# Performance work log

Hardware: AMD Instinct MI355X
Metric: run time of the kernel (lower is better)

Reference implementation:

```python
import jax, jax.numpy as jnp
import numpy as np

B, S, DM, H, DK, DV = 2, 2048, 1024, 16, 64, 64

def setup_inputs() -> dict:
    key = jax.random.key(0)
    ks = jax.random.split(key, 12)
    s = 0.02
    return {
        "Q": jax.random.normal(ks[0], (B, S, DM), jnp.float32),
        "K": jax.random.normal(ks[1], (B, S, DM), jnp.float32),
        "V": jax.random.normal(ks[2], (B, S, DM), jnp.float32),
        "mask": jax.random.randint(ks[3], (B, S, S), 0, 2).astype(bool),
        "wq": jax.random.normal(ks[4], (DM, H * DK), jnp.float32) * s,
        "bq": jnp.zeros((H * DK,), jnp.float32),
        "wk": jax.random.normal(ks[5], (DM, H * DK), jnp.float32) * s,
        "bk": jnp.zeros((H * DK,), jnp.float32),
        "wv": jax.random.normal(ks[6], (DM, H * DV), jnp.float32) * s,
        "bv": jnp.zeros((H * DV,), jnp.float32),
        "wo": jax.random.normal(ks[7], (H * DV, DM), jnp.float32) * s,
        "bo": jnp.zeros((DM,), jnp.float32),
    }

def reference(Q, K, V, mask, wq, bq, wk, bk, wv, bv, wo, bo):
    b = Q.shape[0]
    # projections -> [b, h, s, d]
    q = (Q @ wq + bq).reshape(b, -1, H, DK).transpose(0, 2, 1, 3)
    k = (K @ wk + bk).reshape(b, -1, H, DK).transpose(0, 2, 1, 3)
    v = (V @ wv + bv).reshape(b, -1, H, DV).transpose(0, 2, 1, 3)
    # scaled dot-product attention with boolean mask (True = masked out)
    scores = jnp.einsum("bhqd,bhkd->bhqk", q, k) / jnp.sqrt(jnp.float32(DK))
    scores = jnp.where(mask[:, None, :, :], jnp.float32(-1e9), scores)
    attn = jax.nn.softmax(scores, axis=-1)  # [b,h,s,s]
    ctx = jnp.einsum("bhqk,bhkd->bhqd", attn, v)
    ctx = ctx.transpose(0, 2, 1, 3).reshape(b, -1, H * DV)
    out = ctx @ wo + bo  # [b, s, d_model]
    return out, attn
```

## Files before the change

### kernel.cpp

```cpp
#include <hip/hip_runtime.h>

typedef unsigned short u16;
typedef unsigned int u32;
typedef unsigned long long u64;
typedef __attribute__((ext_vector_type(8))) short bf16x8;
typedef __attribute__((ext_vector_type(4))) float f32x4;

#define NB 2
#define NS 2048
#define NDM 1024
#define NH 16

#define MFMA_B16(a, b, c) __builtin_amdgcn_mfma_f32_16x16x32_bf16(a, b, c, 0, 0, 0)

__device__ __forceinline__ u16 f2bf(float f) {
  union { float f; unsigned u; } v; v.f = f;
  return (u16)((v.u + 0x7fffu + ((v.u >> 16) & 1u)) >> 16);
}
__device__ __forceinline__ float bf2f(u16 h) {
  union { float f; unsigned u; } v; v.u = ((u32)h) << 16; return v.f;
}

__global__ __launch_bounds__(256) void cast3_bf16(const float* __restrict__ a,
                                                  const float* __restrict__ b,
                                                  const float* __restrict__ c,
                                                  u16* __restrict__ oa, u16* __restrict__ ob,
                                                  u16* __restrict__ oc) {
  int i = blockIdx.x * 256 + threadIdx.x;
  const float* src; u16* dst; int j;
  if (i < 1048576) { src = a; dst = oa; j = i; }
  else if (i < 2097152) { src = b; dst = ob; j = i - 1048576; }
  else { src = c; dst = oc; j = i - 2097152; }
  const float4 v = reinterpret_cast<const float4*>(src)[j];
  ushort4 o; o.x = f2bf(v.x); o.y = f2bf(v.y); o.z = f2bf(v.z); o.w = f2bf(v.w);
  reinterpret_cast<ushort4*>(dst)[j] = o;
}

struct TW4 { const float* in[4]; u16* out[4]; };
__global__ __launch_bounds__(256) void transpose_w4(TW4 tw) {
  __shared__ float tile[32][33];
  const float* in = tw.in[blockIdx.z];
  u16* out = tw.out[blockIdx.z];
  int bx = blockIdx.x, by = blockIdx.y;
  int x = threadIdx.x & 31, y0 = threadIdx.x >> 5;
#pragma unroll
  for (int i = 0; i < 4; i++) {
    int y = y0 + i * 8;
    tile[y][x] = in[(by * 32 + y) * NDM + bx * 32 + x];
  }
  __syncthreads();
#pragma unroll
  for (int i = 0; i < 4; i++) {
    int y = y0 + i * 8;
    out[(bx * 32 + y) * NDM + by * 32 + x] = f2bf(tile[x][y]);
  }
}

__global__ __launch_bounds__(256) void mask2bits(const u32* __restrict__ mask, u32* __restrict__ mb) {
  int idx = blockIdx.x * 256 + threadIdx.x;
  u32 mw0 = mask[threadIdx.x & 63];
  bool floatmode = (__ballot(mw0 == 0x3F800000u) != 0ull);
  bool bytemode = !floatmode && (__ballot((mw0 >> 8) != 0u) != 0ull);
  int row = idx >> 6;
  int wword = idx & 63;
  u32 bits = 0;
  if (!bytemode) {
    const uint4* p = reinterpret_cast<const uint4*>(mask + (size_t)row * 2048 + wword * 32);
#pragma unroll
    for (int i = 0; i < 8; i++) {
      uint4 v = p[i];
      bits |= (v.x ? 1u : 0u) << (i * 4 + 0);
      bits |= (v.y ? 1u : 0u) << (i * 4 + 1);
      bits |= (v.z ? 1u : 0u) << (i * 4 + 2);
      bits |= (v.w ? 1u : 0u) << (i * 4 + 3);
    }
  } else {
    const uint4* p = reinterpret_cast<const uint4*>(
        reinterpret_cast<const unsigned char*>(mask) + (size_t)row * 2048 + wword * 32);
#pragma unroll
    for (int i = 0; i < 2; i++) {
      uint4 v = p[i];
      u32 wsv[4] = {v.x, v.y, v.z, v.w};
#pragma unroll
      for (int j = 0; j < 4; j++)
#pragma unroll
        for (int kq = 0; kq < 4; kq++)
          bits |= ((((wsv[j] >> (kq * 8)) & 0xffu) != 0u) ? 1u : 0u) << (i * 16 + j * 4 + kq);
    }
  }
  mb[idx] = bits;
}

struct GArgs { const u16* X; const u16* W; const float* bias; void* out; int mode; float scale; };

__global__ __launch_bounds__(256, 2) void gemm_bt(GArgs g0, GArgs g1, GArgs g2) {
  GArgs ga = (blockIdx.z == 0) ? g0 : (blockIdx.z == 1 ? g1 : g2);
  const int K = 1024, N = 1024;
  __shared__ u16 As[128 * 32];
  __shared__ u16 Bs[128 * 32];
  const int t = threadIdx.x, w = t >> 6, l = t & 63;
  const int m0 = blockIdx.x * 128, n0 = blockIdx.y * 128;
  const int wm = (w >> 1) * 64, wn = (w & 1) * 64;
  const f32x4 fz = {0.f, 0.f, 0.f, 0.f};
  f32x4 acc[4][4];
#pragma unroll
  for (int i = 0; i < 4; i++)
#pragma unroll
    for (int j = 0; j < 4; j++) acc[i][j] = fz;

  for (int k0 = 0; k0 < K; k0 += 32) {
#pragma unroll
    for (int i = 0; i < 2; i++) {
      int idx = i * 256 + w * 64 + l;
      int r = idx >> 2, c = (idx & 3) * 8;
      __builtin_amdgcn_global_load_lds(
          reinterpret_cast<const unsigned*>(ga.X + (size_t)(m0 + r) * K + k0 + c),
          reinterpret_cast<unsigned*>(&As[(i * 256 + w * 64) * 8]), 16, 0, 0);
      __builtin_amdgcn_global_load_lds(
          reinterpret_cast<const unsigned*>(ga.W + (size_t)(n0 + r) * K + k0 + c),
          reinterpret_cast<unsigned*>(&Bs[(i * 256 + w * 64) * 8]), 16, 0, 0);
    }
    __syncthreads();
    bf16x8 af[4], bfr[4];
#pragma unroll
    for (int mt = 0; mt < 4; mt++)
      af[mt] = *reinterpret_cast<const bf16x8*>(&As[(wm + mt * 16 + (l & 15)) * 32 + (l >> 4) * 8]);
#pragma unroll
    for (int nt = 0; nt < 4; nt++)
      bfr[nt] = *reinterpret_cast<const bf16x8*>(&Bs[(wn + nt * 16 + (l & 15)) * 32 + (l >> 4) * 8]);
#pragma unroll
    for (int mt = 0; mt < 4; mt++)
#pragma unroll
      for (int nt = 0; nt < 4; nt++)
        acc[mt][nt] = MFMA_B16(af[mt], bfr[nt], acc[mt][nt]);
    __syncthreads();
  }

#pragma unroll
  for (int nt = 0; nt < 4; nt++) {
    int n = n0 + wn + nt * 16 + (l & 15);
    float bias = ga.bias[n];
#pragma unroll
    for (int mt = 0; mt < 4; mt++) {
      int mb = m0 + wm + mt * 16 + ((l >> 4) << 2);
#pragma unroll
      for (int r = 0; r < 4; r++) {
        int m = mb + r;
        float v = (acc[mt][nt][r] + bias) * ga.scale;
        if (ga.mode == 2) {
          reinterpret_cast<float*>(ga.out)[(size_t)m * N + n] = v;
        } else {
          int b = m >> 11, s = m & 2047, h = n >> 6, d = n & 63;
          if (ga.mode == 0)
            reinterpret_cast<u16*>(ga.out)[(((size_t)(b * NH + h) * NS + s) << 6) + d] = f2bf(v);
          else
            reinterpret_cast<u16*>(ga.out)[((size_t)(b * NH + h) * 64 + d) * NS + s] = f2bf(v);
        }
      }
    }
  }
}

__global__ __launch_bounds__(256, 4) void attn_kernel(
    const u16* __restrict__ qh, const u16* __restrict__ kh, const u16* __restrict__ vT,
    const u32* __restrict__ mb, float* __restrict__ attn, u16* __restrict__ ctx) {
  __shared__ u16 Ks[2][32 * 64];
  __shared__ u16 Vs[3][64 * 32];
  __shared__ u16 Ps[4][2][16 * 40];
  const int tid = threadIdx.x, w = tid >> 6, l = tid & 63;
  int id = blockIdx.x;
  int wgid = (id & 7) * 128 + (id >> 3);
  int qt = wgid & 31, pr = wgid >> 5;
  int h = pr & 15, b = pr >> 4;
  const size_t head = (size_t)b * NH + h;
  const u16* qp = qh + head * NS * 64;
  const u16* kp = kh + head * NS * 64;
  const u16* vp = vT + head * 64 * NS;
  const int qr0 = qt * 64 + w * 16;
  const int lo = l & 15, hi = l >> 4;
  const int rbase = hi << 2;
  const f32x4 fz = {0.f, 0.f, 0.f, 0.f};

  bf16x8 aq0, aq1;
  {
    const u16* p = qp + (size_t)(qr0 + lo) * 64 + hi * 8;
    aq0 = *reinterpret_cast<const bf16x8*>(p);
    aq1 = *reinterpret_cast<const bf16x8*>(p + 32);
  }
  const u32* mrow = mb + ((size_t)b * NS + qr0 + rbase) * 64;

  const int k_row = tid >> 3, k_slot = tid & 7;
  const u16* ksrc0 = kp + (size_t)k_row * 64 + ((k_slot ^ (k_row & 7)) * 8);
  const int v_dv = tid >> 2, v_slot = tid & 3;
  const u16* vsrc0 = vp + (size_t)v_dv * NS + ((v_slot ^ ((v_dv >> 1) & 3)) * 8);
  const int sxk = lo & 7;
  const int sxv = (lo >> 1) & 3;

#define STAGE_KT(tt, bi)                                                                \
  __builtin_amdgcn_global_load_lds(                                                     \
      reinterpret_cast<const unsigned*>(ksrc0 + (size_t)(tt) * 2048),                   \
      reinterpret_cast<unsigned*>(&Ks[bi][w * 512]), 16, 0, 0);
#define STAGE_VT(tt, bi)                                                                \
  __builtin_amdgcn_global_load_lds(                                                     \
      reinterpret_cast<const unsigned*>(vsrc0 + (size_t)(tt) * 32),                     \
      reinterpret_cast<unsigned*>(&Vs[bi][w * 512]), 16, 0, 0);

#define QK_TILE(kb, s0, s1)                                                             \
  {                                                                                     \
    const u16* kbase = &Ks[kb][0];                                                      \
    bf16x8 b00 = *reinterpret_cast<const bf16x8*>(&kbase[(lo) * 64 + ((hi ^ sxk) * 8)]);        \
    bf16x8 b01 = *reinterpret_cast<const bf16x8*>(&kbase[(lo) * 64 + (((4 + hi) ^ sxk) * 8)]);  \
    bf16x8 b10 = *reinterpret_cast<const bf16x8*>(&kbase[(16 + lo) * 64 + ((hi ^ sxk) * 8)]);   \
    bf16x8 b11 = *reinterpret_cast<const bf16x8*>(&kbase[(16 + lo) * 64 + (((4 + hi) ^ sxk) * 8)]); \
    s0 = MFMA_B16(aq1, b01, MFMA_B16(aq0, b00, fz));                                    \
    s1 = MFMA_B16(aq1, b11, MFMA_B16(aq0, b10, fz));                                    \
  }
#define EXP_PS(pb, s0, s1)                                                              \
  {                                                                                     \
    u16* pc = &Ps[w][pb][0];                                                            \
    float p;                                                                            \
    p = ((mc0 >> lo) & 1u) ? 0.f : __expf(s0[0]) * rs0; pc[(rbase + 0) * 40 + lo] = f2bf(p); \
    p = ((mc1 >> lo) & 1u) ? 0.f : __expf(s0[1]) * rs1; pc[(rbase + 1) * 40 + lo] = f2bf(p); \
    p = ((mc2 >> lo) & 1u) ? 0.f : __expf(s0[2]) * rs2; pc[(rbase + 2) * 40 + lo] = f2bf(p); \
    p = ((mc3 >> lo) & 1u) ? 0.f : __expf(s0[3]) * rs3; pc[(rbase + 3) * 40 + lo] = f2bf(p); \
    int bit1 = 16 + lo;                                                                 \
    p = ((mc0 >> bit1) & 1u) ? 0.f : __expf(s1[0]) * rs0; pc[(rbase + 0) * 40 + 16 + lo] = f2bf(p); \
    p = ((mc1 >> bit1) & 1u) ? 0.f : __expf(s1[1]) * rs1; pc[(rbase + 1) * 40 + 16 + lo] = f2bf(p); \
    p = ((mc2 >> bit1) & 1u) ? 0.f : __expf(s1[2]) * rs2; pc[(rbase + 2) * 40 + 16 + lo] = f2bf(p); \
    p = ((mc3 >> bit1) & 1u) ? 0.f : __expf(s1[3]) * rs3; pc[(rbase + 3) * 40 + 16 + lo] = f2bf(p); \
  }
#define PV_STORES(tt, pb, vb)                                                           \
  {                                                                                     \
    u16* pp = &Ps[w][pb][0];                                                            \
    const u16* vbase = &Vs[vb][0];                                                      \
    bf16x8 pa = *reinterpret_cast<const bf16x8*>(&pp[lo * 40 + hi * 8]);                \
    bf16x8 v0 = *reinterpret_cast<const bf16x8*>(&vbase[(lo) * 32 + ((hi ^ sxv) * 8)]);        \
    bf16x8 v1 = *reinterpret_cast<const bf16x8*>(&vbase[(16 + lo) * 32 + ((hi ^ sxv) * 8)]);   \
    bf16x8 v2 = *reinterpret_cast<const bf16x8*>(&vbase[(32 + lo) * 32 + ((hi ^ sxv) * 8)]);   \
    bf16x8 v3 = *reinterpret_cast<const bf16x8*>(&vbase[(48 + lo) * 32 + ((hi ^ sxv) * 8)]);   \
    c0 = MFMA_B16(pa, v0, c0);                                                          \
    c1 = MFMA_B16(pa, v1, c1);                                                          \
    c2 = MFMA_B16(pa, v2, c2);                                                          \
    c3 = MFMA_B16(pa, v3, c3);                                                          \
    float* arow = abase + (size_t)srow * NS + (tt) * 32 + schunk * 8;                   \
    bf16x8 q0 = *reinterpret_cast<const bf16x8*>(&pp[srow * 40 + schunk * 8]);          \
    f32x4 o0, o1;                                                                       \
    _Pragma("unroll") for (int j = 0; j < 4; ++j) {                                     \
      o0[j] = bf2f((u16)q0[j]); o1[j] = bf2f((u16)q0[j + 4]);                           \
    }                                                                                   \
    *reinterpret_cast<f32x4*>(arow + 0) = o0;                                           \
    *reinterpret_cast<f32x4*>(arow + 4) = o1;                                           \
  }

  float rs0 = 0.f, rs1 = 0.f, rs2 = 0.f, rs3 = 0.f;

  u32 mc0 = mrow[0], mc1 = mrow[64], mc2 = mrow[128], mc3 = mrow[192];
  STAGE_KT(0, 0);
  asm volatile("s_waitcnt vmcnt(0)" ::: "memory");
  __builtin_amdgcn_s_barrier();
  asm volatile("" ::: "memory");

  for (int t = 0; t < 64; ++t) {
    STAGE_KT(t + 1, (t + 1) & 1);
    u32 mn0 = mrow[t + 1], mn1 = mrow[65 + t], mn2 = mrow[129 + t], mn3 = mrow[193 + t];
    asm volatile("" ::: "memory");
    f32x4 s0, s1;
    QK_TILE(t & 1, s0, s1);
    rs0 += ((mc0 >> lo) & 1u) ? 0.f : __expf(s0[0]);
    rs1 += ((mc1 >> lo) & 1u) ? 0.f : __expf(s0[1]);
    rs2 += ((mc2 >> lo) & 1u) ? 0.f : __expf(s0[2]);
    rs3 += ((mc3 >> lo) & 1u) ? 0.f : __expf(s0[3]);
    int bit1 = 16 + lo;
    rs0 += ((mc0 >> bit1) & 1u) ? 0.f : __expf(s1[0]);
    rs1 += ((mc1 >> bit1) & 1u) ? 0.f : __expf(s1[1]);
    rs2 += ((mc2 >> bit1) & 1u) ? 0.f : __expf(s1[2]);
    rs3 += ((mc3 >> bit1) & 1u) ? 0.f : __expf(s1[3]);
    mc0 = mn0; mc1 = mn1; mc2 = mn2; mc3 = mn3;
    asm volatile("s_waitcnt vmcnt(4)" ::: "memory");
    __builtin_amdgcn_s_barrier();
    asm volatile("" ::: "memory");
  }

  {
    float v;
    v = rs0; v += __shfl_xor(v, 1); v += __shfl_xor(v, 2); v += __shfl_xor(v, 4); v += __shfl_xor(v, 8);
    rs0 = 1.f / fmaxf(v, 1e-30f);
    v = rs1; v += __shfl_xor(v, 1); v += __shfl_xor(v, 2); v += __shfl_xor(v, 4); v += __shfl_xor(v, 8);
    rs1 = 1.f / fmaxf(v, 1e-30f);
    v = rs2; v += __shfl_xor(v, 1); v += __shfl_xor(v, 2); v += __shfl_xor(v, 4); v += __shfl_xor(v, 8);
    rs2 = 1.f / fmaxf(v, 1e-30f);
    v = rs3; v += __shfl_xor(v, 1); v += __shfl_xor(v, 2); v += __shfl_xor(v, 4); v += __shfl_xor(v, 8);
    rs3 = 1.f / fmaxf(v, 1e-30f);
  }

  f32x4 c0 = fz, c1 = fz, c2 = fz, c3 = fz;
  float* abase = attn + (head * NS + qr0) * NS;
  const int srow = l >> 2, schunk = l & 3;

  mc0 = mrow[0]; mc1 = mrow[64]; mc2 = mrow[128]; mc3 = mrow[192];
  STAGE_KT(0, 0);
  STAGE_VT(0, 0);
  asm volatile("s_waitcnt vmcnt(0)" ::: "memory");
  __builtin_amdgcn_s_barrier();
  asm volatile("" ::: "memory");

  {
    STAGE_KT(1, 1);
    STAGE_VT(1, 1);
    u32 mn0 = mrow[1], mn1 = mrow[65], mn2 = mrow[129], mn3 = mrow[193];
    asm volatile("" ::: "memory");
    f32x4 s0, s1;
    QK_TILE(0, s0, s1);
    EXP_PS(0, s0, s1);
    mc0 = mn0; mc1 = mn1; mc2 = mn2; mc3 = mn3;
    asm volatile("s_waitcnt vmcnt(4)" ::: "memory");
    __builtin_amdgcn_s_barrier();
    asm volatile("" ::: "memory");
  }

  for (int t = 1; t < 64; ++t) {
    if (t + 1 < 64) {
      int vb2 = (t + 1) % 3;
      STAGE_KT(t + 1, (t + 1) & 1);
      STAGE_VT(t + 1, vb2);
    }
    u32 mn0 = mrow[t + 1], mn1 = mrow[65 + t], mn2 = mrow[129 + t], mn3 = mrow[193 + t];
    asm volatile("" ::: "memory");
    PV_STORES(t - 1, (t - 1) & 1, (t - 1) % 3);
    f32x4 s0, s1;
    QK_TILE(t & 1, s0, s1);
    EXP_PS(t & 1, s0, s1);
    mc0 = mn0; mc1 = mn1; mc2 = mn2; mc3 = mn3;
    asm volatile("s_waitcnt vmcnt(6)" ::: "memory");
    __builtin_amdgcn_s_barrier();
    asm volatile("" ::: "memory");
  }

  PV_STORES(63, 1, 0);

#define CTXW(cv, ct)                                                                      \
  {                                                                                       \
    ctx[((size_t)b * NS + qr0 + rbase + 0) * 1024 + h * 64 + (ct)*16 + lo] = f2bf(cv[0]); \
    ctx[((size_t)b * NS + qr0 + rbase + 1) * 1024 + h * 64 + (ct)*16 + lo] = f2bf(cv[1]); \
    ctx[((size_t)b * NS + qr0 + rbase + 2) * 1024 + h * 64 + (ct)*16 + lo] = f2bf(cv[2]); \
    ctx[((size_t)b * NS + qr0 + rbase + 3) * 1024 + h * 64 + (ct)*16 + lo] = f2bf(cv[3]); \
  }
  CTXW(c0, 0) CTXW(c1, 1) CTXW(c2, 2) CTXW(c3, 3)
#undef CTXW
#undef STAGE_KT
#undef STAGE_VT
#undef QK_TILE
#undef EXP_PS
#undef PV_STORES
}

extern "C" void kernel_launch(void* const* d_in, const int* in_sizes, int n_in,
                              void* d_out, int out_size, void* d_ws, size_t ws_size,
                              hipStream_t stream) {
  const float* Q = (const float*)d_in[0];
  const float* K = (const float*)d_in[1];
  const float* V = (const float*)d_in[2];
  const u32* mask = (const u32*)d_in[3];
  const float* wq = (const float*)d_in[4];
  const float* bq = (const float*)d_in[5];
  const float* wk = (const float*)d_in[6];
  const float* bk = (const float*)d_in[7];
  const float* wv = (const float*)d_in[8];
  const float* bv = (const float*)d_in[9];
  const float* wo = (const float*)d_in[10];
  const float* bo = (const float*)d_in[11];
  float* out = (float*)d_out;
  float* attn = out + (size_t)NB * NS * NDM;

  char* ws = (char*)d_ws;
  u16* Qb  = (u16*)(ws + 0);
  u16* Kb  = (u16*)(ws + 8388608);
  u16* Vb  = (u16*)(ws + 16777216);
  u16* wqT = (u16*)(ws + 25165824);
  u16* wkT = (u16*)(ws + 27262976);
  u16* wvT = (u16*)(ws + 29360128);
  u16* woT = (u16*)(ws + 31457280);
  u16* qhd = (u16*)(ws + 33554432);
  u16* khd = (u16*)(ws + 41943040);
  u16* vTd = (u16*)(ws + 50331648);
  u16* ctx = (u16*)(ws + 58720256);
  u32* mbits = (u32*)(ws + 0);

  cast3_bf16<<<12288, 256, 0, stream>>>(Q, K, V, Qb, Kb, Vb);
  TW4 tw;
  tw.in[0] = wq; tw.in[1] = wk; tw.in[2] = wv; tw.in[3] = wo;
  tw.out[0] = wqT; tw.out[1] = wkT; tw.out[2] = wvT; tw.out[3] = woT;
  transpose_w4<<<dim3(32, 32, 4), 256, 0, stream>>>(tw);

  GArgs gq = {Qb, wqT, bq, (void*)qhd, 0, 0.125f};
  GArgs gk = {Kb, wkT, bk, (void*)khd, 0, 1.0f};
  GArgs gv = {Vb, wvT, bv, (void*)vTd, 1, 1.0f};
  gemm_bt<<<dim3(32, 8, 3), 256, 0, stream>>>(gq, gk, gv);

  mask2bits<<<1024, 256, 0, stream>>>(mask, mbits);

  attn_kernel<<<1024, 256, 0, stream>>>(qhd, khd, vTd, mbits, attn, ctx);

  GArgs go = {ctx, woT, bo, d_out, 2, 1.0f};
  gemm_bt<<<dim3(32, 8, 1), 256, 0, stream>>>(go, go, go);
}
```

Measured before the change: 330.4 us.

## Split attention row-sum pass into separate kernel with key-halved parallelism

Moves the first softmax pass (QK^T, exp, masked row-sum) out of the fused attention kernel into its own kernel. That kernel splits the keys into two halves and launches twice as many workgroups with higher occupancy. Partial sums go to workspace and the second kernel combines them before normalizing and writing attn and ctx. This aims to raise parallelism and occupancy for the row-sum phase, at the cost of an extra launch and recomputing Q loads and mask reads.

```diff
diff --git a/kernel.cpp b/kernel.cpp
--- a/kernel.cpp
+++ b/kernel.cpp
@@ -161,9 +161,101 @@
   }
 }
 
-__global__ __launch_bounds__(256, 4) void attn_kernel(
+__global__ __launch_bounds__(256, 6) void attn_rowsum(
+    const u16* __restrict__ qh, const u16* __restrict__ kh,
+    const u32* __restrict__ mb, float* __restrict__ psums) {
+  __shared__ u16 Ks[2][32 * 64];
+  const int tid = threadIdx.x, w = tid >> 6, l = tid & 63;
+  int id = blockIdx.x;
+  int wgid = (id & 7) * 256 + (id >> 3);
+  int pr = wgid >> 6, r6 = wgid & 63;
+  int qt = r6 >> 1, half = r6 & 1;
+  int h = pr & 15, b = pr >> 4;
+  const size_t head = (size_t)b * NH + h;
+  const u16* qp = qh + head * NS * 64;
+  const u16* kp = kh + head * NS * 64;
+  const int qr0 = qt * 64 + w * 16;
+  const int lo = l & 15, hi = l >> 4;
+  const int rbase = hi << 2;
+  const f32x4 fz = {0.f, 0.f, 0.f, 0.f};
+
+  bf16x8 aq0, aq1;
+  {
+    const u16* p = qp + (size_t)(qr0 + lo) * 64 + hi * 8;
+    aq0 = *reinterpret_cast<const bf16x8*>(p);
+    aq1 = *reinterpret_cast<const bf16x8*>(p + 32);
+  }
+  const u32* mrow = mb + ((size_t)b * NS + qr0 + rbase) * 64 + half * 32;
+
+  const int k_row = tid >> 3, k_slot = tid & 7;
+  const u16* ksrc0 = kp + (size_t)(half * 1024) * 64 + (size_t)k_row * 64 +
+                     ((k_slot ^ (k_row & 7)) * 8);
+  const int sxk = lo & 7;
+
+#define STAGE_KT(tt)                                                                    \
+  __builtin_amdgcn_global_load_lds(                                                     \
+      reinterpret_cast<const unsigned*>(ksrc0 + (size_t)(tt) * 2048),                   \
+      reinterpret_cast<unsigned*>(&Ks[(tt) & 1][w * 512]), 16, 0, 0);
+
+  float rs0 = 0.f, rs1 = 0.f, rs2 = 0.f, rs3 = 0.f;
+
+  u32 mc0 = mrow[0], mc1 = mrow[64], mc2 = mrow[128], mc3 = mrow[192];
+  STAGE_KT(0);
+  asm volatile("s_waitcnt vmcnt(0)" ::: "memory");
+  __builtin_amdgcn_s_barrier();
+  asm volatile("" ::: "memory");
+
+  for (int t = 0; t < 32; ++t) {
+    STAGE_KT(t + 1);
+    u32 mn0 = mrow[t + 1], mn1 = mrow[65 + t], mn2 = mrow[129 + t], mn3 = mrow[193 + t];
+    asm volatile("" ::: "memory");
+    const u16* kbase = &Ks[t & 1][0];
+    bf16x8 b00 = *reinterpret_cast<const bf16x8*>(&kbase[(lo) * 64 + ((hi ^ sxk) * 8)]);
+    bf16x8 b01 = *reinterpret_cast<const bf16x8*>(&kbase[(lo) * 64 + (((4 + hi) ^ sxk) * 8)]);
+    bf16x8 b10 = *reinterpret_cast<const bf16x8*>(&kbase[(16 + lo) * 64 + ((hi ^ sxk) * 8)]);
+    bf16x8 b11 = *reinterpret_cast<const bf16x8*>(&kbase[(16 + lo) * 64 + (((4 + hi) ^ sxk) * 8)]);
+    f32x4 s0 = MFMA_B16(aq1, b01, MFMA_B16(aq0, b00, fz));
+    f32x4 s1 = MFMA_B16(aq1, b11, MFMA_B16(aq0, b10, fz));
+    rs0 += ((mc0 >> lo) & 1u) ? 0.f : __expf(s0[0]);
+    rs1 += ((mc1 >> lo) & 1u) ? 0.f : __expf(s0[1]);
+    rs2 += ((mc2 >> lo) & 1u) ? 0.f : __expf(s0[2]);
+    rs3 += ((mc3 >> lo) & 1u) ? 0.f : __expf(s0[3]);
+    int bit1 = 16 + lo;
+    rs0 += ((mc0 >> bit1) & 1u) ? 0.f : __expf(s1[0]);
+    rs1 += ((mc1 >> bit1) & 1u) ? 0.f : __expf(s1[1]);
+    rs2 += ((mc2 >> bit1) & 1u) ? 0.f : __expf(s1[2]);
+    rs3 += ((mc3 >> bit1) & 1u) ? 0.f : __expf(s1[3]);
+    mc0 = mn0; mc1 = mn1; mc2 = mn2; mc3 = mn3;
+    asm volatile("s_waitcnt vmcnt(4)" ::: "memory");
+    __builtin_amdgcn_s_barrier();
+    asm volatile("" ::: "memory");
+  }
+#undef STAGE_KT
+
+  {
+    float v;
+    v = rs0; v += __shfl_xor(v, 1); v += __shfl_xor(v, 2); v += __shfl_xor(v, 4); v += __shfl_xor(v, 8);
+    rs0 = v;
+    v = rs1; v += __shfl_xor(v, 1); v += __shfl_xor(v, 2); v += __shfl_xor(v, 4); v += __shfl_xor(v, 8);
+    rs1 = v;
+    v = rs2; v += __shfl_xor(v, 1); v += __shfl_xor(v, 2); v += __shfl_xor(v, 4); v += __shfl_xor(v, 8);
+    rs2 = v;
+    v = rs3; v += __shfl_xor(v, 1); v += __shfl_xor(v, 2); v += __shfl_xor(v, 4); v += __shfl_xor(v, 8);
+    rs3 = v;
+  }
+  if (lo == 0) {
+    size_t base = (head * NS + qr0 + rbase) * 2 + half;
+    psums[base + 0] = rs0;
+    psums[base + 2] = rs1;
+    psums[base + 4] = rs2;
+    psums[base + 6] = rs3;
+  }
+}
+
+__global__ __launch_bounds__(256, 4) void attn_pass2(
     const u16* __restrict__ qh, const u16* __restrict__ kh, const u16* __restrict__ vT,
-    const u32* __restrict__ mb, float* __restrict__ attn, u16* __restrict__ ctx) {
+    const u32* __restrict__ mb, const float* __restrict__ psums,
+    float* __restrict__ attn, u16* __restrict__ ctx) {
   __shared__ u16 Ks[2][32 * 64];
   __shared__ u16 Vs[3][64 * 32];
   __shared__ u16 Ps[4][2][16 * 40];
@@ -188,6 +280,16 @@
     aq1 = *reinterpret_cast<const bf16x8*>(p + 32);
   }
   const u32* mrow = mb + ((size_t)b * NS + qr0 + rbase) * 64;
+
+  float rs0, rs1, rs2, rs3;
+  {
+    const float2* pb = reinterpret_cast<const float2*>(psums) + (head * NS + qr0 + rbase);
+    float2 q0 = pb[0], q1 = pb[1], q2 = pb[2], q3 = pb[3];
+    rs0 = 1.f / fmaxf(q0.x + q0.y, 1e-30f);
+    rs1 = 1.f / fmaxf(q1.x + q1.y, 1e-30f);
+    rs2 = 1.f / fmaxf(q2.x + q2.y, 1e-30f);
+    rs3 = 1.f / fmaxf(q3.x + q3.y, 1e-30f);
+  }
 
   const int k_row = tid >> 3, k_slot = tid & 7;
   const u16* ksrc0 = kp + (size_t)k_row * 64 + ((k_slot ^ (k_row & 7)) * 8);
@@ -252,52 +354,11 @@
     *reinterpret_cast<f32x4*>(arow + 4) = o1;                                           \
   }
 
-  float rs0 = 0.f, rs1 = 0.f, rs2 = 0.f, rs3 = 0.f;
-
-  u32 mc0 = mrow[0], mc1 = mrow[64], mc2 = mrow[128], mc3 = mrow[192];
-  STAGE_KT(0, 0);
-  asm volatile("s_waitcnt vmcnt(0)" ::: "memory");
-  __builtin_amdgcn_s_barrier();
-  asm volatile("" ::: "memory");
-
-  for (int t = 0; t < 64; ++t) {
-    STAGE_KT(t + 1, (t + 1) & 1);
-    u32 mn0 = mrow[t + 1], mn1 = mrow[65 + t], mn2 = mrow[129 + t], mn3 = mrow[193 + t];
-    asm volatile("" ::: "memory");
-    f32x4 s0, s1;
-    QK_TILE(t & 1, s0, s1);
-    rs0 += ((mc0 >> lo) & 1u) ? 0.f : __expf(s0[0]);
-    rs1 += ((mc1 >> lo) & 1u) ? 0.f : __expf(s0[1]);
-    rs2 += ((mc2 >> lo) & 1u) ? 0.f : __expf(s0[2]);
-    rs3 += ((mc3 >> lo) & 1u) ? 0.f : __expf(s0[3]);
-    int bit1 = 16 + lo;
-    rs0 += ((mc0 >> bit1) & 1u) ? 0.f : __expf(s1[0]);
-    rs1 += ((mc1 >> bit1) & 1u) ? 0.f : __expf(s1[1]);
-    rs2 += ((mc2 >> bit1) & 1u) ? 0.f : __expf(s1[2]);
-    rs3 += ((mc3 >> bit1) & 1u) ? 0.f : __expf(s1[3]);
-    mc0 = mn0; mc1 = mn1; mc2 = mn2; mc3 = mn3;
-    asm volatile("s_waitcnt vmcnt(4)" ::: "memory");
-    __builtin_amdgcn_s_barrier();
-    asm volatile("" ::: "memory");
-  }
-
-  {
-    float v;
-    v = rs0; v += __shfl_xor(v, 1); v += __shfl_xor(v, 2); v += __shfl_xor(v, 4); v += __shfl_xor(v, 8);
-    rs0 = 1.f / fmaxf(v, 1e-30f);
-    v = rs1; v += __shfl_xor(v, 1); v += __shfl_xor(v, 2); v += __shfl_xor(v, 4); v += __shfl_xor(v, 8);
-    rs1 = 1.f / fmaxf(v, 1e-30f);
-    v = rs2; v += __shfl_xor(v, 1); v += __shfl_xor(v, 2); v += __shfl_xor(v, 4); v += __shfl_xor(v, 8);
-    rs2 = 1.f / fmaxf(v, 1e-30f);
-    v = rs3; v += __shfl_xor(v, 1); v += __shfl_xor(v, 2); v += __shfl_xor(v, 4); v += __shfl_xor(v, 8);
-    rs3 = 1.f / fmaxf(v, 1e-30f);
-  }
-
   f32x4 c0 = fz, c1 = fz, c2 = fz, c3 = fz;
   float* abase = attn + (head * NS + qr0) * NS;
   const int srow = l >> 2, schunk = l & 3;
 
-  mc0 = mrow[0]; mc1 = mrow[64]; mc2 = mrow[128]; mc3 = mrow[192];
+  u32 mc0 = mrow[0], mc1 = mrow[64], mc2 = mrow[128], mc3 = mrow[192];
   STAGE_KT(0, 0);
   STAGE_VT(0, 0);
   asm volatile("s_waitcnt vmcnt(0)" ::: "memory");
@@ -385,6 +446,7 @@
   u16* vTd = (u16*)(ws + 50331648);
   u16* ctx = (u16*)(ws + 58720256);
   u32* mbits = (u32*)(ws + 0);
+  float* psums = (float*)(ws + 1048576);
 
   cast3_bf16<<<12288, 256, 0, stream>>>(Q, K, V, Qb, Kb, Vb);
   TW4 tw;
@@ -399,7 +461,8 @@
 
   mask2bits<<<1024, 256, 0, stream>>>(mask, mbits);
 
-  attn_kernel<<<1024, 256, 0, stream>>>(qhd, khd, vTd, mbits, attn, ctx);
+  attn_rowsum<<<2048, 256, 0, stream>>>(qhd, khd, mbits, psums);
+  attn_pass2<<<1024, 256, 0, stream>>>(qhd, khd, vTd, mbits, psums, attn, ctx);
 
   GArgs go = {ctx, woT, bo, d_out, 2, 1.0f};
   gemm_bt<<<dim3(32, 8, 1), 256, 0, stream>>>(go, go, go);
```

New measurement: 332.0 us. About the same (+0.5%).
